# Performance work log

Hardware: AMD Instinct MI355X
Metric: run time of the kernel (lower is better)

## Reference

```python
import jax, jax.numpy as jnp
import numpy as np


def setup_inputs() -> dict:
    key = jax.random.key(0)
    k = jax.random.split(key, 6)
    B, S, d, n = 4, 4096, 1024, 64
    x = jax.random.normal(k[0], (B, S, d), dtype=jnp.float32)
    gate_W = jax.random.normal(k[1], (d, n), dtype=jnp.float32) / np.sqrt(d).astype(np.float32)
    gate_b = jnp.full((n,), 3.0, dtype=jnp.float32)  # nn.init.constant_(gate_proj.bias, 3.0)
    B_W = jax.random.normal(k[2], (d, n), dtype=jnp.float32) / np.sqrt(d).astype(np.float32)
    C_W = jax.random.normal(k[3], (n, d), dtype=jnp.float32) / np.sqrt(n).astype(np.float32)
    out_W = jax.random.normal(k[4], (d, d), dtype=jnp.float32) / np.sqrt(d).astype(np.float32)
    mix_weight = jnp.eye(n, dtype=jnp.float32) + 0.01 * jax.random.normal(k[5], (n, n), dtype=jnp.float32)
    return {"x": x, "gate_W": gate_W, "gate_b": gate_b, "B_W": B_W,
            "C_W": C_W, "out_W": out_W, "mix_weight": mix_weight, "chunk_size": 16}


def _ssm_forward(x, gate_W, gate_b, B_W, C_W, out_W, mix_weight, chunk_size):
    Bb, S, d = x.shape
    n = gate_W.shape[1]
    C = chunk_size
    K = S // C  # seq_len chosen divisible by chunk_size -> F.pad path is a no-op
    # Vectorized per-timestep projections (done once for the whole sequence)
    gates = jax.nn.sigmoid(jnp.einsum('bsd,dn->bsn', x, gate_W) + gate_b)  # a_t in (0,1)
    b_all = jnp.einsum('bsd,dn->bsn', x, B_W)
    a_ch = gates.reshape(Bb, K, C, n).transpose(1, 2, 0, 3)  # (K, C, B, n)
    b_ch = b_all.reshape(Bb, K, C, n).transpose(1, 2, 0, 3)

    def chunk_step(h_prev, ab):
        a_c, b_c = ab  # each (C, B, n)
        def step(h, t):
            a_t, b_t = t
            h = a_t * h + b_t
            return h, h
        h_final, h_stack = jax.lax.scan(step, h_prev, (a_c, b_c))  # h_stack: (C, B, n)
        gate_prod = jnp.prod(a_c, axis=0)  # (B, n) cumulative diag gates
        # T_chunk = mix @ diag(gate_prod): T[b,i,j] = mix[i,j] * gate_prod[b,j]
        T = mix_weight[None, :, :] * gate_prod[:, None, :]
        Th = jnp.einsum('bij,bj->bi', T, h_prev)
        b_chunk = h_final - Th
        h_next = Th + b_chunk  # canonical inter-chunk propagation: T @ h_prev + b_chunk
        return h_next, h_stack

    h0 = jnp.zeros((Bb, n), dtype=x.dtype)
    _, h_all = jax.lax.scan(chunk_step, h0, (a_ch, b_ch))  # (K, C, B, n)
    h_seq = h_all.transpose(2, 0, 1, 3).reshape(Bb, S, n)
    y = jnp.einsum('bsn,nd->bsd', h_seq, C_W)
    out_gate = jax.nn.sigmoid(jnp.einsum('bsd,de->bse', x, out_W))
    return y * out_gate


def reference(x, gate_W, gate_b, B_W, C_W, out_W, mix_weight, chunk_size):
    return _ssm_forward(x, gate_W, gate_b, B_W, C_W, out_W, mix_weight, chunk_size)
```

## Files before the change

kernel.cpp:

```cpp
#include <hip/hip_runtime.h>
#include <stdint.h>

typedef __attribute__((ext_vector_type(8))) short short8;
typedef __attribute__((ext_vector_type(4))) float f32x4;
typedef __attribute__((ext_vector_type(4))) float f4;
typedef __attribute__((ext_vector_type(4))) unsigned short us4;

typedef unsigned short ushort_t;

__device__ __forceinline__ ushort_t f2bf(float f) {
    union { float f; uint32_t u; } c; c.f = f;
    uint32_t u = c.u;
    uint32_t r = u + 0x7fffu + ((u >> 16) & 1u);
    return (ushort_t)(r >> 16);
}
__device__ __forceinline__ float bf2f(ushort_t h) {
    union { uint32_t u; float f; } c; c.u = ((uint32_t)h) << 16;
    return c.f;
}

typedef const __attribute__((address_space(1))) unsigned int as1_uint;
typedef __attribute__((address_space(3))) unsigned int as3_uint;
__device__ __forceinline__ void gload_lds16(const void* g, void* l) {
    __builtin_amdgcn_global_load_lds((as1_uint*)g, (as3_uint*)l, 16, 0, 0);
}

#define SWIDX(r, c) ((r) * 64 + ((c) ^ (((r) & 7) << 3)))

__global__ void prep_weights(const float* __restrict__ gate_W, const float* __restrict__ B_W,
                             const float* __restrict__ C_W, const float* __restrict__ out_W,
                             ushort_t* __restrict__ W1t_hi, ushort_t* __restrict__ W1t_lo,
                             ushort_t* __restrict__ outWt, ushort_t* __restrict__ Ct)
{
    int idx = blockIdx.x * 256 + threadIdx.x;
    int stride = gridDim.x * 256;
    for (int i = idx; i < 1024 * 1024; i += stride) {
        int nn = i >> 10, kk = i & 1023;
        outWt[i] = f2bf(out_W[kk * 1024 + nn]);
    }
    for (int i = idx; i < 128 * 1024; i += stride) {
        int nn = i >> 10, kk = i & 1023;
        float v = (nn < 64) ? gate_W[kk * 64 + nn] : B_W[kk * 64 + (nn - 64)];
        ushort_t h = f2bf(v);
        W1t_hi[i] = h;
        W1t_lo[i] = f2bf(v - bf2f(h));
    }
    for (int i = idx; i < 1024 * 64; i += stride) {
        int nn = i >> 6, kk = i & 63;
        Ct[i] = f2bf(C_W[kk * 1024 + nn]);
    }
}

__global__ __launch_bounds__(256, 2)
void p1_kernel(const float* __restrict__ x,
               const ushort_t* __restrict__ W1t_hi, const ushort_t* __restrict__ W1t_lo,
               ushort_t* __restrict__ x_hi, float* __restrict__ Zpart)
{
    __shared__ ushort_t Ash[128 * 64];
    __shared__ ushort_t Asl[128 * 64];
    __shared__ ushort_t Bsh[64 * 64];
    __shared__ ushort_t Bsl[64 * 64];

    const int tid = threadIdx.x;
    const int wave = tid >> 6, lane = tid & 63;
    const int wm = wave >> 1, wn = wave & 1;
    const int s0 = blockIdx.x * 64;
    const int kc = blockIdx.y;

    f32x4 acc[4][2];
#pragma unroll
    for (int i = 0; i < 4; i++)
#pragma unroll
        for (int j = 0; j < 2; j++) { f32x4 z = {0.f,0.f,0.f,0.f}; acc[i][j] = z; }

    for (int kt = 0; kt < 8; ++kt) {
        const int k0 = kc * 512 + kt * 64;
#pragma unroll
        for (int p = 0; p < 4; ++p) {
            int c = p * 256 + wave * 64 + lane;
            int row = c >> 3, col = (c & 7) * 8;
            gload_lds16(W1t_hi + (size_t)row * 1024 + k0 + col,
                        &Ash[(p * 256 + wave * 64) * 8]);
            gload_lds16(W1t_lo + (size_t)row * 1024 + k0 + col,
                        &Asl[(p * 256 + wave * 64) * 8]);
        }
#pragma unroll
        for (int p = 0; p < 4; ++p) {
            int f = tid + p * 256;
            int row = f >> 4, col = (f & 15) * 4;
            f4 v = *(const f4*)(x + (size_t)(s0 + row) * 1024 + k0 + col);
            us4 hi, lo;
#pragma unroll
            for (int j = 0; j < 4; j++) {
                ushort_t h = f2bf(v[j]);
                hi[j] = h;
                lo[j] = f2bf(v[j] - bf2f(h));
            }
            *(us4*)&Bsh[row * 64 + col] = hi;
            *(us4*)&Bsl[row * 64 + col] = lo;
            *(us4*)(x_hi + (size_t)(s0 + row) * 1024 + k0 + col) = hi;
        }
        __syncthreads();
#pragma unroll
        for (int kk = 0; kk < 2; ++kk) {
            const int kb = kk * 32 + (lane >> 4) * 8;
            short8 ah[4], al[4], bh[2], bl[2];
#pragma unroll
            for (int fm = 0; fm < 4; fm++) {
                int r = wm * 64 + fm * 16 + (lane & 15);
                ah[fm] = *(const short8*)&Ash[r * 64 + kb];
                al[fm] = *(const short8*)&Asl[r * 64 + kb];
            }
#pragma unroll
            for (int fn = 0; fn < 2; fn++) {
                int r = wn * 32 + fn * 16 + (lane & 15);
                bh[fn] = *(const short8*)&Bsh[r * 64 + kb];
                bl[fn] = *(const short8*)&Bsl[r * 64 + kb];
            }
#pragma unroll
            for (int fm = 0; fm < 4; fm++)
#pragma unroll
                for (int fn = 0; fn < 2; fn++) {
                    acc[fm][fn] = __builtin_amdgcn_mfma_f32_16x16x32_bf16(ah[fm], bh[fn], acc[fm][fn], 0, 0, 0);
                    acc[fm][fn] = __builtin_amdgcn_mfma_f32_16x16x32_bf16(al[fm], bh[fn], acc[fm][fn], 0, 0, 0);
                    acc[fm][fn] = __builtin_amdgcn_mfma_f32_16x16x32_bf16(ah[fm], bl[fn], acc[fm][fn], 0, 0, 0);
                }
        }
        __syncthreads();
    }
#pragma unroll
    for (int fm = 0; fm < 4; fm++) {
#pragma unroll
        for (int fn = 0; fn < 2; fn++) {
            int scol = s0 + wn * 32 + fn * 16 + (lane & 15);
            int b = scol >> 12, sb = scol & 4095;
            int nbase = wm * 64 + fm * 16 + ((lane >> 4) << 2);
#pragma unroll
            for (int r = 0; r < 4; r++) {
                Zpart[((size_t)kc * 512 + b * 128 + nbase + r) * 4096 + sb] = acc[fm][fn][r];
            }
        }
    }
}

__global__ __launch_bounds__(256)
void scan_kernel(const float* __restrict__ Zpart, const float* __restrict__ gate_b,
                 ushort_t* __restrict__ hT)
{
    __shared__ float SA[256], SB[256];
    const int bn = blockIdx.x;
    const int t = threadIdx.x;
    const int b = bn >> 6, n = bn & 63;
    const float gb = gate_b[n];
    const float* g0 = Zpart + ((size_t)(b * 128 + n)) * 4096;
    const float* g1 = g0 + (size_t)512 * 4096;
    const float* b0 = Zpart + ((size_t)(b * 128 + 64 + n)) * 4096;
    const float* b1 = b0 + (size_t)512 * 4096;
    const int sb = t * 16;

    float a[16], bb[16];
#pragma unroll
    for (int q = 0; q < 4; q++) {
        f4 vg0 = *(const f4*)(g0 + sb + q * 4);
        f4 vg1 = *(const f4*)(g1 + sb + q * 4);
        f4 vb0 = *(const f4*)(b0 + sb + q * 4);
        f4 vb1 = *(const f4*)(b1 + sb + q * 4);
#pragma unroll
        for (int j = 0; j < 4; j++) {
            a[q * 4 + j] = 1.f / (1.f + __expf(-(vg0[j] + vg1[j] + gb)));
            bb[q * 4 + j] = vb0[j] + vb1[j];
        }
    }
    float A = 1.f, Bv = 0.f;
#pragma unroll
    for (int i = 0; i < 16; i++) { Bv = a[i] * Bv + bb[i]; A *= a[i]; }
    SA[t] = A; SB[t] = Bv;
    __syncthreads();
    for (int off = 1; off < 256; off <<= 1) {
        float a1 = 1.f, b1v = 0.f;
        if (t >= off) { a1 = SA[t - off]; b1v = SB[t - off]; }
        float a2 = SA[t], b2 = SB[t];
        __syncthreads();
        SA[t] = a1 * a2;
        SB[t] = a2 * b1v + b2;
        __syncthreads();
    }
    float h = (t == 0) ? 0.f : SB[t - 1];
    ushort_t ov[16];
#pragma unroll
    for (int i = 0; i < 16; i++) {
        h = a[i] * h + bb[i];
        ov[i] = f2bf(h);
    }
    ushort_t* dst = hT + (size_t)bn * 4096 + sb;
#pragma unroll
    for (int q = 0; q < 4; q++) {
        us4 o; o[0]=ov[q*4]; o[1]=ov[q*4+1]; o[2]=ov[q*4+2]; o[3]=ov[q*4+3];
        *(us4*)(dst + q * 4) = o;
    }
}

__global__ __launch_bounds__(512, 2)
void gemm_out256(const ushort_t* __restrict__ x_hi, const ushort_t* __restrict__ outWt,
                 const ushort_t* __restrict__ hT, const ushort_t* __restrict__ Ct,
                 float* __restrict__ out)
{
    __shared__ ushort_t As[2][256 * 64];
    __shared__ ushort_t Bs[2][256 * 64];

    const int tid = threadIdx.x;
    const int wave = tid >> 6, lane = tid & 63;
    const int wm = wave >> 2;
    const int wn = wave & 3;

    const int flat = blockIdx.x;
    const int swz = (flat & 7) * 32 + (flat >> 3);
    const int m0 = (swz >> 2) * 256;
    const int n0 = (swz & 3) * 256;

    const int lcol0 = (lane >> 4) * 8;
    const int lrow = lane & 15;

    f32x4 acc[8][4];
#pragma unroll
    for (int i = 0; i < 8; i++)
#pragma unroll
        for (int j = 0; j < 4; j++) { f32x4 z = {0.f,0.f,0.f,0.f}; acc[i][j] = z; }

    auto stage = [&](int buf, int k0) {
#pragma unroll
        for (int p = 0; p < 4; ++p) {
            int c = p * 512 + wave * 64 + lane;
            int row = c >> 3;
            int col = (((c & 7) ^ (row & 7)) << 3);
            gload_lds16(x_hi + (size_t)(m0 + row) * 1024 + k0 + col,
                        &As[buf][(p * 512 + wave * 64) * 8]);
            gload_lds16(outWt + (size_t)(n0 + row) * 1024 + k0 + col,
                        &Bs[buf][(p * 512 + wave * 64) * 8]);
        }
    };

    stage(0, 0);
    __syncthreads();

    for (int kt = 0; kt < 16; ++kt) {
        if (kt < 15) stage((kt + 1) & 1, (kt + 1) * 64);
        const ushort_t* as = As[kt & 1];
        const ushort_t* bs = Bs[kt & 1];

        short8 bfr[4][2];
#pragma unroll
        for (int fn = 0; fn < 4; fn++)
#pragma unroll
            for (int kk = 0; kk < 2; kk++) {
                int r = wn * 64 + fn * 16 + lrow;
                bfr[fn][kk] = *(const short8*)&bs[SWIDX(r, kk * 32 + lcol0)];
            }
#pragma unroll
        for (int m = 0; m < 8; m++) {
            int r = wm * 128 + m * 16 + lrow;
            short8 a0 = *(const short8*)&as[SWIDX(r, lcol0)];
            short8 a1 = *(const short8*)&as[SWIDX(r, 32 + lcol0)];
#pragma unroll
            for (int fn = 0; fn < 4; fn++) {
                acc[m][fn] = __builtin_amdgcn_mfma_f32_16x16x32_bf16(a0, bfr[fn][0], acc[m][fn], 0, 0, 0);
                acc[m][fn] = __builtin_amdgcn_mfma_f32_16x16x32_bf16(a1, bfr[fn][1], acc[m][fn], 0, 0, 0);
            }
        }
        __syncthreads();
    }

    const int b64 = (m0 >> 12) * 64;
    const int sb0 = m0 & 4095;
#pragma unroll
    for (int p = 0; p < 4; ++p) {
        int c = p * 512 + wave * 64 + lane;
        int row = c >> 3;
        int col = (((c & 7) ^ (row & 7)) << 3);
        gload_lds16(Ct + (size_t)(n0 + row) * 64 + col,
                    &Bs[0][(p * 512 + wave * 64) * 8]);
    }
#pragma unroll
    for (int p = 0; p < 4; ++p) {
        int c = tid + p * 512;
        int kn = c >> 5, mc = c & 31;
        short8 v = *(const short8*)(hT + (size_t)(b64 + kn) * 4096 + sb0 + mc * 8);
#pragma unroll
        for (int j = 0; j < 8; ++j)
            As[0][SWIDX(mc * 8 + j, kn)] = (ushort_t)v[j];
    }
    __syncthreads();

    short8 by[4][2];
#pragma unroll
    for (int fn = 0; fn < 4; fn++)
#pragma unroll
        for (int kk = 0; kk < 2; kk++) {
            int r = wn * 64 + fn * 16 + lrow;
            by[fn][kk] = *(const short8*)&Bs[0][SWIDX(r, kk * 32 + lcol0)];
        }

#pragma unroll
    for (int g = 0; g < 4; g++) {
        f32x4 ty[2][4];
#pragma unroll
        for (int mm = 0; mm < 2; mm++)
#pragma unroll
            for (int fn = 0; fn < 4; fn++) { f32x4 z = {0.f,0.f,0.f,0.f}; ty[mm][fn] = z; }
#pragma unroll
        for (int mm = 0; mm < 2; mm++) {
            int r = wm * 128 + (g * 2 + mm) * 16 + lrow;
            short8 a0 = *(const short8*)&As[0][SWIDX(r, lcol0)];
            short8 a1 = *(const short8*)&As[0][SWIDX(r, 32 + lcol0)];
#pragma unroll
            for (int fn = 0; fn < 4; fn++) {
                ty[mm][fn] = __builtin_amdgcn_mfma_f32_16x16x32_bf16(a0, by[fn][0], ty[mm][fn], 0, 0, 0);
                ty[mm][fn] = __builtin_amdgcn_mfma_f32_16x16x32_bf16(a1, by[fn][1], ty[mm][fn], 0, 0, 0);
            }
        }
#pragma unroll
        for (int mm = 0; mm < 2; mm++)
#pragma unroll
            for (int fn = 0; fn < 4; fn++) {
                int col = n0 + wn * 64 + fn * 16 + lrow;
                int rbase = m0 + wm * 128 + (g * 2 + mm) * 16 + ((lane >> 4) << 2);
#pragma unroll
                for (int r = 0; r < 4; r++) {
                    float og = 1.f / (1.f + __expf(-acc[g * 2 + mm][fn][r]));
                    out[(size_t)(rbase + r) * 1024 + col] = ty[mm][fn][r] * og;
                }
            }
    }
}

extern "C" void kernel_launch(void* const* d_in, const int* in_sizes, int n_in,
                              void* d_out, int out_size, void* d_ws, size_t ws_size,
                              hipStream_t stream)
{
    const float* x      = (const float*)d_in[0];
    const float* gate_W = (const float*)d_in[1];
    const float* gate_b = (const float*)d_in[2];
    const float* B_W    = (const float*)d_in[3];
    const float* C_W    = (const float*)d_in[4];
    const float* out_W  = (const float*)d_in[5];
    float* out = (float*)d_out;

    char* ws = (char*)d_ws;
    float*    Zpart  = (float*)(ws + 0);
    ushort_t* hT     = (ushort_t*)(ws + 16777216);
    ushort_t* x_hi   = (ushort_t*)(ws + 18874368);
    ushort_t* W1t_hi = (ushort_t*)(ws + 52428800);
    ushort_t* W1t_lo = (ushort_t*)(ws + 52690944);
    ushort_t* outWt  = (ushort_t*)(ws + 52953088);
    ushort_t* Ct     = (ushort_t*)(ws + 55050240);

    prep_weights<<<512, 256, 0, stream>>>(gate_W, B_W, C_W, out_W,
                                          W1t_hi, W1t_lo, outWt, Ct);

    p1_kernel<<<dim3(256, 2), 256, 0, stream>>>(x, W1t_hi, W1t_lo, x_hi, Zpart);

    scan_kernel<<<256, 256, 0, stream>>>(Zpart, gate_b, hT);

    gemm_out256<<<256, 512, 0, stream>>>(x_hi, outWt, hT, Ct, out);
}
```

Measured before the change: 98.97 us.

## Interleave half-tile global loads with MFMA phases using fine-grained barriers and priority

The main out_W GEMM k-loop is split into four sub-phases per k-tile, each issuing one quarter of the next tile's global-to-LDS loads while computing two M-fragments of MFMAs. Explicit s_barrier, waitcnt, sched_barrier and s_setprio calls stagger waves so memory and matrix work overlap, instead of bulk staging followed by one __syncthreads. This adds more barriers per tile and relies on hand-placed waitcnts being correct for the double buffer.

```diff
diff --git a/kernel.cpp b/kernel.cpp
--- a/kernel.cpp
+++ b/kernel.cpp
@@ -227,47 +227,67 @@
 #pragma unroll
         for (int j = 0; j < 4; j++) { f32x4 z = {0.f,0.f,0.f,0.f}; acc[i][j] = z; }
 
-    auto stage = [&](int buf, int k0) {
-#pragma unroll
-        for (int p = 0; p < 4; ++p) {
-            int c = p * 512 + wave * 64 + lane;
-            int row = c >> 3;
+    auto stage_half = [&](int buf, int k0, int ht) {
+        const ushort_t* src = (ht < 2) ? x_hi : outWt;
+        const int base0 = (ht < 2) ? m0 : n0;
+        const int rh = (ht & 1) * 128;
+        ushort_t* lds = (ht < 2) ? &As[buf][0] : &Bs[buf][0];
+#pragma unroll
+        for (int i = 0; i < 2; ++i) {
+            int c = i * 512 + wave * 64 + lane;
+            int row = rh + (c >> 3);
             int col = (((c & 7) ^ (row & 7)) << 3);
-            gload_lds16(x_hi + (size_t)(m0 + row) * 1024 + k0 + col,
-                        &As[buf][(p * 512 + wave * 64) * 8]);
-            gload_lds16(outWt + (size_t)(n0 + row) * 1024 + k0 + col,
-                        &Bs[buf][(p * 512 + wave * 64) * 8]);
+            gload_lds16(src + (size_t)(base0 + row) * 1024 + k0 + col,
+                        lds + rh * 64 + (i * 512 + wave * 64) * 8);
         }
     };
 
-    stage(0, 0);
-    __syncthreads();
-
-    for (int kt = 0; kt < 16; ++kt) {
-        if (kt < 15) stage((kt + 1) & 1, (kt + 1) * 64);
-        const ushort_t* as = As[kt & 1];
-        const ushort_t* bs = Bs[kt & 1];
-
-        short8 bfr[4][2];
-#pragma unroll
-        for (int fn = 0; fn < 4; fn++)
-#pragma unroll
-            for (int kk = 0; kk < 2; kk++) {
-                int r = wn * 64 + fn * 16 + lrow;
-                bfr[fn][kk] = *(const short8*)&bs[SWIDX(r, kk * 32 + lcol0)];
-            }
-#pragma unroll
-        for (int m = 0; m < 8; m++) {
-            int r = wm * 128 + m * 16 + lrow;
-            short8 a0 = *(const short8*)&as[SWIDX(r, lcol0)];
-            short8 a1 = *(const short8*)&as[SWIDX(r, 32 + lcol0)];
-#pragma unroll
-            for (int fn = 0; fn < 4; fn++) {
-                acc[m][fn] = __builtin_amdgcn_mfma_f32_16x16x32_bf16(a0, bfr[fn][0], acc[m][fn], 0, 0, 0);
-                acc[m][fn] = __builtin_amdgcn_mfma_f32_16x16x32_bf16(a1, bfr[fn][1], acc[m][fn], 0, 0, 0);
-            }
-        }
-        __syncthreads();
+#pragma unroll
+    for (int ht = 0; ht < 4; ++ht) stage_half(0, 0, ht);
+    asm volatile("s_waitcnt vmcnt(0)" ::: "memory");
+    __builtin_amdgcn_s_barrier();
+
+    short8 bfr[4][2];
+    for (int t = 0; t < 16; ++t) {
+        const int buf = t & 1;
+        const ushort_t* as = As[buf];
+        const ushort_t* bs = Bs[buf];
+#pragma unroll
+        for (int q = 0; q < 4; ++q) {
+            if (t < 15) stage_half(buf ^ 1, (t + 1) * 64, q);
+            short8 afr[2][2];
+#pragma unroll
+            for (int mm = 0; mm < 2; ++mm) {
+                int r = wm * 128 + (2 * q + mm) * 16 + lrow;
+                afr[mm][0] = *(const short8*)&as[SWIDX(r, lcol0)];
+                afr[mm][1] = *(const short8*)&as[SWIDX(r, 32 + lcol0)];
+            }
+            if (q == 0) {
+#pragma unroll
+                for (int fn = 0; fn < 4; fn++)
+#pragma unroll
+                    for (int kk = 0; kk < 2; kk++) {
+                        int r = wn * 64 + fn * 16 + lrow;
+                        bfr[fn][kk] = *(const short8*)&bs[SWIDX(r, kk * 32 + lcol0)];
+                    }
+            }
+            __builtin_amdgcn_s_barrier();
+            asm volatile("s_waitcnt lgkmcnt(0)" ::: "memory");
+            __builtin_amdgcn_sched_barrier(0);
+            __builtin_amdgcn_s_setprio(1);
+#pragma unroll
+            for (int mm = 0; mm < 2; ++mm)
+#pragma unroll
+                for (int fn = 0; fn < 4; ++fn) {
+                    acc[2 * q + mm][fn] = __builtin_amdgcn_mfma_f32_16x16x32_bf16(
+                        afr[mm][0], bfr[fn][0], acc[2 * q + mm][fn], 0, 0, 0);
+                    acc[2 * q + mm][fn] = __builtin_amdgcn_mfma_f32_16x16x32_bf16(
+                        afr[mm][1], bfr[fn][1], acc[2 * q + mm][fn], 0, 0, 0);
+                }
+            __builtin_amdgcn_s_setprio(0);
+            if (q == 3) asm volatile("s_waitcnt vmcnt(0)" ::: "memory");
+            __builtin_amdgcn_s_barrier();
+        }
     }
 
     const int b64 = (m0 >> 12) * 64;
```

After: 101.7 us. 1.03x slower.

## Pipeline out-gate GEMM main loop with quarter-tile staged loads and wave priority

Applied to the files above, without the earlier changes.

Restructures the 256x256 bf16 MFMA main loop of the out-gate GEMM into four quarter phases per K-step. Each phase issues a partial global-to-LDS load for a future buffer, prefetches the next A fragments from LDS, and raises wave priority around its MFMA burst. The fixed full-tile stage followed by __syncthreads is replaced with fine-grained vmcnt waits and s_barriers. The M-row-to-wave mapping is interleaved so each quarter covers a contiguous 64-row slab, and the epilogue is updated to match. This aims to overlap memory traffic with MFMA work, at the cost of complex hand-tuned wait counts that are easy to get wrong.

```diff
diff --git a/kernel.cpp b/kernel.cpp
--- a/kernel.cpp
+++ b/kernel.cpp
@@ -220,6 +220,29 @@
 
     const int lcol0 = (lane >> 4) * 8;
     const int lrow = lane & 15;
+    const int lxor = (lrow & 7) << 3;
+
+    const int aOff0 = (wm * 32 + lrow) * 64 + (lcol0 ^ lxor);
+    const int aOff1 = (wm * 32 + lrow) * 64 + ((32 + lcol0) ^ lxor);
+    const int bOff0 = (wn * 64 + lrow) * 64 + (lcol0 ^ lxor);
+    const int bOff1 = (wn * 64 + lrow) * 64 + ((32 + lcol0) ^ lxor);
+
+    const int rl0 = tid >> 3;
+    const int col0 = ((tid & 7) ^ (rl0 & 7)) << 3;
+    const ushort_t* gB0a = outWt + (size_t)(n0 + rl0) * 1024 + col0;
+    const ushort_t* gB0b = gB0a + 64 * 1024;
+    const ushort_t* gB1a = outWt + (size_t)(n0 + 128 + rl0) * 1024 + col0;
+    const ushort_t* gB1b = gB1a + 64 * 1024;
+    const ushort_t* gA0a = x_hi + (size_t)(m0 + rl0) * 1024 + col0;
+    const ushort_t* gA0b = gA0a + 64 * 1024;
+    const ushort_t* gA1a = x_hi + (size_t)(m0 + 128 + rl0) * 1024 + col0;
+    const ushort_t* gA1b = gA1a + 64 * 1024;
+
+    auto STG = [&](const ushort_t*& ga, const ushort_t*& gb, ushort_t* ldsbase) {
+        gload_lds16(ga, ldsbase + wave * 512);
+        gload_lds16(gb, ldsbase + 4096 + wave * 512);
+        ga += 64; gb += 64;
+    };
 
     f32x4 acc[8][4];
 #pragma unroll
@@ -227,48 +250,102 @@
 #pragma unroll
         for (int j = 0; j < 4; j++) { f32x4 z = {0.f,0.f,0.f,0.f}; acc[i][j] = z; }
 
-    auto stage = [&](int buf, int k0) {
-#pragma unroll
-        for (int p = 0; p < 4; ++p) {
-            int c = p * 512 + wave * 64 + lane;
-            int row = c >> 3;
-            int col = (((c & 7) ^ (row & 7)) << 3);
-            gload_lds16(x_hi + (size_t)(m0 + row) * 1024 + k0 + col,
-                        &As[buf][(p * 512 + wave * 64) * 8]);
-            gload_lds16(outWt + (size_t)(n0 + row) * 1024 + k0 + col,
-                        &Bs[buf][(p * 512 + wave * 64) * 8]);
-        }
-    };
-
-    stage(0, 0);
-    __syncthreads();
-
-    for (int kt = 0; kt < 16; ++kt) {
-        if (kt < 15) stage((kt + 1) & 1, (kt + 1) * 64);
-        const ushort_t* as = As[kt & 1];
-        const ushort_t* bs = Bs[kt & 1];
-
+    STG(gB0a, gB0b, &Bs[0][0]);
+    STG(gB1a, gB1b, &Bs[0][8192]);
+    STG(gA0a, gA0b, &As[0][0]);
+    STG(gA1a, gA1b, &As[0][8192]);
+    STG(gB0a, gB0b, &Bs[1][0]);
+    STG(gB1a, gB1b, &Bs[1][8192]);
+    STG(gA0a, gA0b, &As[1][0]);
+    asm volatile("s_waitcnt vmcnt(6)" ::: "memory");
+    __builtin_amdgcn_s_barrier();
+
+    short8 aF[2][2], aN[2][2];
+#pragma unroll
+    for (int mm = 0; mm < 2; ++mm) {
+        aF[mm][0] = *(const short8*)&As[0][aOff0 + mm * 1024];
+        aF[mm][1] = *(const short8*)&As[0][aOff1 + mm * 1024];
+    }
+
+#define MFMA_Q(q)                                                                  \
+    do {                                                                           \
+        __builtin_amdgcn_s_setprio(1);                                             \
+        _Pragma("unroll") for (int mm = 0; mm < 2; ++mm)                           \
+            _Pragma("unroll") for (int fn = 0; fn < 4; ++fn) {                     \
+                acc[2*(q)+mm][fn] = __builtin_amdgcn_mfma_f32_16x16x32_bf16(       \
+                    aF[mm][0], bfr[fn][0], acc[2*(q)+mm][fn], 0, 0, 0);            \
+                acc[2*(q)+mm][fn] = __builtin_amdgcn_mfma_f32_16x16x32_bf16(       \
+                    aF[mm][1], bfr[fn][1], acc[2*(q)+mm][fn], 0, 0, 0);            \
+            }                                                                      \
+        __builtin_amdgcn_s_setprio(0);                                             \
+    } while (0)
+
+#define ACOPY()                                                                    \
+    do { aF[0][0]=aN[0][0]; aF[0][1]=aN[0][1]; aF[1][0]=aN[1][0]; aF[1][1]=aN[1][1]; } while (0)
+
+    for (int t = 0; t < 16; ++t) {
+        const int bc = t & 1;
+        const ushort_t* aP0 = &As[bc][aOff0];
+        const ushort_t* aP1 = &As[bc][aOff1];
+        const ushort_t* bP0 = &Bs[bc][bOff0];
+        const ushort_t* bP1 = &Bs[bc][bOff1];
+        const ushort_t* nA0 = &As[bc ^ 1][aOff0];
+        const ushort_t* nA1 = &As[bc ^ 1][aOff1];
         short8 bfr[4][2];
-#pragma unroll
-        for (int fn = 0; fn < 4; fn++)
-#pragma unroll
-            for (int kk = 0; kk < 2; kk++) {
-                int r = wn * 64 + fn * 16 + lrow;
-                bfr[fn][kk] = *(const short8*)&bs[SWIDX(r, kk * 32 + lcol0)];
-            }
-#pragma unroll
-        for (int m = 0; m < 8; m++) {
-            int r = wm * 128 + m * 16 + lrow;
-            short8 a0 = *(const short8*)&as[SWIDX(r, lcol0)];
-            short8 a1 = *(const short8*)&as[SWIDX(r, 32 + lcol0)];
-#pragma unroll
-            for (int fn = 0; fn < 4; fn++) {
-                acc[m][fn] = __builtin_amdgcn_mfma_f32_16x16x32_bf16(a0, bfr[fn][0], acc[m][fn], 0, 0, 0);
-                acc[m][fn] = __builtin_amdgcn_mfma_f32_16x16x32_bf16(a1, bfr[fn][1], acc[m][fn], 0, 0, 0);
-            }
-        }
-        __syncthreads();
-    }
+
+        __builtin_amdgcn_s_barrier();
+        if (t < 15) STG(gA1a, gA1b, &As[bc ^ 1][8192]);
+#pragma unroll
+        for (int fn = 0; fn < 4; ++fn) {
+            bfr[fn][0] = *(const short8*)(bP0 + fn * 1024);
+            bfr[fn][1] = *(const short8*)(bP1 + fn * 1024);
+        }
+#pragma unroll
+        for (int mm = 0; mm < 2; ++mm) {
+            aN[mm][0] = *(const short8*)(aP0 + 4096 + mm * 1024);
+            aN[mm][1] = *(const short8*)(aP1 + 4096 + mm * 1024);
+        }
+        MFMA_Q(0);
+        ACOPY();
+
+        if (t < 15) { asm volatile("s_waitcnt vmcnt(8)" ::: "memory"); }
+        else        { asm volatile("s_waitcnt vmcnt(0)" ::: "memory"); }
+        __builtin_amdgcn_s_barrier();
+        if (t < 14) STG(gB0a, gB0b, &Bs[bc][0]);
+#pragma unroll
+        for (int mm = 0; mm < 2; ++mm) {
+            aN[mm][0] = *(const short8*)(aP0 + 2 * 4096 + mm * 1024);
+            aN[mm][1] = *(const short8*)(aP1 + 2 * 4096 + mm * 1024);
+        }
+        MFMA_Q(1);
+        ACOPY();
+
+        __builtin_amdgcn_s_barrier();
+        if (t < 14) STG(gB1a, gB1b, &Bs[bc][8192]);
+#pragma unroll
+        for (int mm = 0; mm < 2; ++mm) {
+            aN[mm][0] = *(const short8*)(aP0 + 3 * 4096 + mm * 1024);
+            aN[mm][1] = *(const short8*)(aP1 + 3 * 4096 + mm * 1024);
+        }
+        MFMA_Q(2);
+        ACOPY();
+
+        if (t < 14)       { asm volatile("s_waitcnt vmcnt(6)" ::: "memory"); }
+        else if (t == 14) { asm volatile("s_waitcnt vmcnt(2)" ::: "memory"); }
+        __builtin_amdgcn_s_barrier();
+        if (t < 14) STG(gA0a, gA0b, &As[bc][0]);
+        if (t < 15) {
+#pragma unroll
+            for (int mm = 0; mm < 2; ++mm) {
+                aN[mm][0] = *(const short8*)(nA0 + mm * 1024);
+                aN[mm][1] = *(const short8*)(nA1 + mm * 1024);
+            }
+        }
+        MFMA_Q(3);
+        if (t < 15) ACOPY();
+    }
+#undef MFMA_Q
+#undef ACOPY
 
     const int b64 = (m0 >> 12) * 64;
     const int sb0 = m0 & 4095;
@@ -309,7 +386,7 @@
             for (int fn = 0; fn < 4; fn++) { f32x4 z = {0.f,0.f,0.f,0.f}; ty[mm][fn] = z; }
 #pragma unroll
         for (int mm = 0; mm < 2; mm++) {
-            int r = wm * 128 + (g * 2 + mm) * 16 + lrow;
+            int r = g * 64 + wm * 32 + mm * 16 + lrow;
             short8 a0 = *(const short8*)&As[0][SWIDX(r, lcol0)];
             short8 a1 = *(const short8*)&As[0][SWIDX(r, 32 + lcol0)];
 #pragma unroll
@@ -323,7 +400,7 @@
 #pragma unroll
             for (int fn = 0; fn < 4; fn++) {
                 int col = n0 + wn * 64 + fn * 16 + lrow;
-                int rbase = m0 + wm * 128 + (g * 2 + mm) * 16 + ((lane >> 4) << 2);
+                int rbase = m0 + g * 64 + wm * 32 + mm * 16 + ((lane >> 4) << 2);
 #pragma unroll
                 for (int r = 0; r < 4; r++) {
                     float og = 1.f / (1.f + __expf(-acc[g * 2 + mm][fn][r]));
```

After: 99.55 us. About the same (+0.6%).
